# Kernel tuning notes

Measured on AMD Instinct MI355X. Metric: run time of the kernel, lower is better.

## Reference

```python
import jax, jax.numpy as jnp
import numpy as np

N = 20000      # total nodes
E = 320000     # edges (before self loops)
B = 8          # graphs in batch
F_IN = 100
HID = 256
HEADS = 4
DIMS = [(256, 256), (256, 128), (128, 64), (64, 32)]  # (in_dim, out_dim) per level
NEG_SLOPE = 0.2
LN_EPS = 1e-5


def _glorot(k, shape):
    fan = shape[0] + shape[-1]
    return jax.random.normal(k, shape, jnp.float32) * jnp.sqrt(2.0 / fan)


def setup_inputs() -> dict:
    key = jax.random.key(0)
    ks = jax.random.split(key, 32)
    inp = {}
    inp["x"] = jax.random.normal(ks[0], (N, F_IN), jnp.float32)
    inp["edge_index"] = jax.random.randint(ks[1], (2, E), 0, N)
    inp["batch"] = jnp.sort(jax.random.randint(ks[2], (N,), 0, B))
    inp["W_in"] = _glorot(ks[3], (F_IN, HID))
    inp["b_in"] = jnp.zeros((HID,), jnp.float32)
    i = 4
    for l, (di, do) in enumerate(DIMS):
        inp[f"W{l}"] = _glorot(ks[i], (di, HEADS * do)); i += 1
        inp[f"as{l}"] = _glorot(ks[i], (HEADS, do)); i += 1
        inp[f"ad{l}"] = _glorot(ks[i], (HEADS, do)); i += 1
        inp[f"b{l}"] = jnp.zeros((do,), jnp.float32)
        inp[f"g{l}"] = jnp.ones((do,), jnp.float32)
        inp[f"be{l}"] = jnp.zeros((do,), jnp.float32)
    inp["W_out"] = _glorot(ks[i], (DIMS[-1][1], 1))
    inp["b_out"] = jnp.zeros((1,), jnp.float32)
    return inp


def _gat(x, src, dst, W, a_s, a_d, b):
    # PyG GATConv, heads=HEADS, concat=False (head mean), bias after mean
    h = (x @ W).reshape(N, HEADS, -1)              # [N,H,C]
    al_s = (h * a_s).sum(-1)                        # [N,H]
    al_d = (h * a_d).sum(-1)                        # [N,H]
    e = jax.nn.leaky_relu(al_s[src] + al_d[dst], NEG_SLOPE)  # [Etot,H]
    m = jax.ops.segment_max(e, dst, num_segments=N)
    m = jnp.where(jnp.isfinite(m), m, 0.0)
    ex = jnp.exp(e - m[dst])
    den = jax.ops.segment_sum(ex, dst, num_segments=N)
    alpha = ex / (den[dst] + 1e-16)                 # segment softmax over incoming edges
    out = jax.ops.segment_sum(alpha[:, :, None] * h[src], dst, num_segments=N)
    return out.mean(axis=1) + b                     # [N,C]


def _ln(x, g, b):
    mu = x.mean(-1, keepdims=True)
    var = ((x - mu) ** 2).mean(-1, keepdims=True)
    return (x - mu) * jax.lax.rsqrt(var + LN_EPS) * g + b


def _forward(x, edge_index, batch, W_in, b_in, level_params, W_out, b_out):
    loop = jnp.arange(N)
    src = jnp.concatenate([edge_index[0], loop])    # add self loops (GATConv default)
    dst = jnp.concatenate([edge_index[1], loop])
    h = jax.nn.relu(x @ W_in + b_in)
    for (di, do), (W, a_s, a_d, b, g, be) in zip(DIMS, level_params):
        out = _gat(h, src, dst, W, a_s, a_d, b)
        out = jax.nn.relu(out)
        out = _ln(out, g, be)
        # dropout is identity in eval mode
        if di == do:
            out = out + h
        h = out
    cnt = jax.ops.segment_sum(jnp.ones((N,), h.dtype), batch, num_segments=B)
    pooled = jax.ops.segment_sum(h, batch, num_segments=B) / jnp.maximum(cnt, 1.0)[:, None]
    return (pooled @ W_out + b_out)[:, 0]           # [B]


def reference(x, edge_index, batch, W_in, b_in,
              W0, as0, ad0, b0, g0, be0,
              W1, as1, ad1, b1, g1, be1,
              W2, as2, ad2, b2, g2, be2,
              W3, as3, ad3, b3, g3, be3,
              W_out, b_out):
    level_params = [
        (W0, as0, ad0, b0, g0, be0),
        (W1, as1, ad1, b1, g1, be1),
        (W2, as2, ad2, b2, g2, be2),
        (W3, as3, ad3, b3, g3, be3),
    ]
    return _forward(x, edge_index, batch, W_in, b_in, level_params, W_out, b_out)
```

## Files before the change

### kernel.cpp

```cpp
#include <hip/hip_runtime.h>
#include <hip/hip_bf16.h>
#include <cstdint>

constexpr int NN   = 20000;
constexpr int NE   = 320000;
constexpr int ETOT = NE + NN;
constexpr int BG   = 8;
constexpr int FIN  = 100;
constexpr int HID  = 256;
constexpr int H    = 4;
constexpr float SLOPE  = 0.2f;
constexpr float LN_EPS = 1e-5f;

#define DEVFN __device__ __forceinline__

typedef __bf16 bf16x8 __attribute__((ext_vector_type(8)));
typedef float  f32x4  __attribute__((ext_vector_type(4)));
typedef float  f32x2  __attribute__((ext_vector_type(2)));

DEVFN float lrelu(float v) { return v > 0.f ? v : SLOPE * v; }
DEVFN ushort f2bf(float f) {
    unsigned u = __float_as_uint(f);
    return (ushort)((u + 0x7fffu + ((u >> 16) & 1u)) >> 16);
}
DEVFN float bf_lo(unsigned u) { return __uint_as_float(u << 16); }
DEVFN float bf_hi(unsigned u) { return __uint_as_float(u & 0xffff0000u); }
DEVFN float bf2f(unsigned u) { return __uint_as_float(u << 16); }

__global__ void zero_u32(uint32_t* __restrict__ p, int n) {
    int i = blockIdx.x * blockDim.x + threadIdx.x;
    if (i < n) p[i] = 0u;
}

__global__ void count_deg(const int* __restrict__ ei, int* __restrict__ deg) {
    int k = blockIdx.x * blockDim.x + threadIdx.x;
    if (k >= ETOT) return;
    int d = (k < NE) ? ei[NE + k] : (k - NE);
    atomicAdd(&deg[d], 1);
}

__global__ void scan_kernel(const int* __restrict__ deg, int* __restrict__ rowptr) {
    __shared__ int buf[1024];
    int carry = 0;
    for (int base = 0; base < NN; base += 1024) {
        int i = base + threadIdx.x;
        int v = (i < NN) ? deg[i] : 0;
        buf[threadIdx.x] = v;
        __syncthreads();
        for (int off = 1; off < 1024; off <<= 1) {
            int t = (threadIdx.x >= off) ? buf[threadIdx.x - off] : 0;
            __syncthreads();
            buf[threadIdx.x] += t;
            __syncthreads();
        }
        int incl = buf[threadIdx.x];
        if (i < NN) rowptr[i] = carry + incl - v;
        int total = buf[1023];
        __syncthreads();
        carry += total;
    }
    if (threadIdx.x == 0) rowptr[NN] = carry;
}

__global__ void scatter_edges(const int* __restrict__ ei, const int* __restrict__ rowptr,
                              int* __restrict__ fill, int* __restrict__ esrc) {
    int k = blockIdx.x * blockDim.x + threadIdx.x;
    if (k >= ETOT) return;
    int s, d;
    if (k < NE) { s = ei[k]; d = ei[NE + k]; }
    else        { s = k - NE; d = k - NE; }
    int pos = rowptr[d] + atomicAdd(&fill[d], 1);
    esrc[pos] = s;
}

template <int KS, int KP, int NC>
__global__ void convW(const float* __restrict__ W, ushort* __restrict__ Wt) {
    int id = blockIdx.x * blockDim.x + threadIdx.x;
    if (id >= NC * KP) return;
    int n = id / KP, k = id - n * KP;
    Wt[id] = (k < KS) ? f2bf(W[(size_t)k * NC + n]) : (ushort)0;
}

__global__ void convX(const float* __restrict__ x, ushort* __restrict__ xpad) {
    int id = blockIdx.x * blockDim.x + threadIdx.x;
    if (id >= NN * 128) return;
    int n = id >> 7, k = id & 127;
    xpad[id] = (k < FIN) ? f2bf(x[(size_t)n * FIN + k]) : (ushort)0;
}

template <int K, int NC, bool BR, bool AL>
__launch_bounds__(256)
__global__ void gemm_mfma(const ushort* __restrict__ A, const ushort* __restrict__ Wt,
                          const float* __restrict__ bias, void* __restrict__ Cout,
                          const float* __restrict__ a_s, const float* __restrict__ a_d,
                          float* __restrict__ al_s, float* __restrict__ al_d, int M) {
    constexpr int LDK = K + 8;
    constexpr int DO_AL = NC / H;
    __shared__ ushort As[64 * LDK];
    __shared__ ushort Bs[64 * LDK];
    const int row0 = blockIdx.x * 64;
    const int col0 = blockIdx.y * 64;
    const int tid = threadIdx.x;
    constexpr int CH = K / 8;
    for (int c = tid; c < 64 * CH; c += 256) {
        int r = c / CH, cc = c - r * CH;
        int gr = row0 + r;
        uint4 v = make_uint4(0u, 0u, 0u, 0u);
        if (gr < M) v = *(const uint4*)(A + (size_t)gr * K + cc * 8);
        *(uint4*)(&As[r * LDK + cc * 8]) = v;
        uint4 w = *(const uint4*)(Wt + (size_t)(col0 + r) * K + cc * 8);
        *(uint4*)(&Bs[r * LDK + cc * 8]) = w;
    }
    __syncthreads();
    const int wave = tid >> 6;
    const int lane = tid & 63;
    const int m = lane & 15;
    const int q = lane >> 4;
    f32x4 acc0 = {0.f, 0.f, 0.f, 0.f}, acc1 = acc0, acc2 = acc0, acc3 = acc0;
    const ushort* ap  = &As[(wave * 16 + m) * LDK + q * 8];
    const ushort* bp0 = &Bs[(0 * 16 + m) * LDK + q * 8];
    const ushort* bp1 = &Bs[(1 * 16 + m) * LDK + q * 8];
    const ushort* bp2 = &Bs[(2 * 16 + m) * LDK + q * 8];
    const ushort* bp3 = &Bs[(3 * 16 + m) * LDK + q * 8];
#pragma unroll
    for (int kk = 0; kk < K / 32; kk++) {
        bf16x8 a = *(const bf16x8*)(ap + kk * 32);
        acc0 = __builtin_amdgcn_mfma_f32_16x16x32_bf16(a, *(const bf16x8*)(bp0 + kk * 32), acc0, 0, 0, 0);
        acc1 = __builtin_amdgcn_mfma_f32_16x16x32_bf16(a, *(const bf16x8*)(bp1 + kk * 32), acc1, 0, 0, 0);
        acc2 = __builtin_amdgcn_mfma_f32_16x16x32_bf16(a, *(const bf16x8*)(bp2 + kk * 32), acc2, 0, 0, 0);
        acc3 = __builtin_amdgcn_mfma_f32_16x16x32_bf16(a, *(const bf16x8*)(bp3 + kk * 32), acc3, 0, 0, 0);
    }
    const int grow0 = row0 + wave * 16 + q * 4;
    if (!AL) {
        ushort* Cb = (ushort*)Cout + (size_t)grow0 * NC + col0 + m;
        float b0 = 0, b1 = 0, b2 = 0, b3 = 0;
        if (BR) {
            b0 = bias[col0 + m];      b1 = bias[col0 + m + 16];
            b2 = bias[col0 + m + 32]; b3 = bias[col0 + m + 48];
        }
#pragma unroll
        for (int r = 0; r < 4; r++) {
            if (grow0 + r < M) {
                float v0 = acc0[r], v1 = acc1[r], v2 = acc2[r], v3 = acc3[r];
                if (BR) {
                    v0 = fmaxf(v0 + b0, 0.f); v1 = fmaxf(v1 + b1, 0.f);
                    v2 = fmaxf(v2 + b2, 0.f); v3 = fmaxf(v3 + b3, 0.f);
                }
                Cb[(size_t)r * NC + 0]  = f2bf(v0);
                Cb[(size_t)r * NC + 16] = f2bf(v1);
                Cb[(size_t)r * NC + 32] = f2bf(v2);
                Cb[(size_t)r * NC + 48] = f2bf(v3);
            }
        }
    } else {
        uchar* Cb = (uchar*)Cout + (size_t)grow0 * NC + col0 + m;
#pragma unroll
        for (int r = 0; r < 4; r++) {
            if (grow0 + r < M) {
                int pk01 = __builtin_amdgcn_cvt_pk_fp8_f32(acc0[r], acc1[r], 0, false);
                int pk23 = __builtin_amdgcn_cvt_pk_fp8_f32(acc2[r], acc3[r], 0, false);
                Cb[(size_t)r * NC + 0]  = (uchar)(pk01 & 0xff);
                Cb[(size_t)r * NC + 16] = (uchar)((pk01 >> 8) & 0xff);
                Cb[(size_t)r * NC + 32] = (uchar)(pk23 & 0xff);
                Cb[(size_t)r * NC + 48] = (uchar)((pk23 >> 8) & 0xff);
            }
        }
        float asv[4], adv[4];
#pragma unroll
        for (int t = 0; t < 4; t++) {
            int gc = col0 + m + 16 * t;
            asv[t] = a_s[gc];
            adv[t] = a_d[gc];
        }
        const int h_lo = col0 / DO_AL;
        const int h_hi = (col0 + 32) / DO_AL;
#pragma unroll
        for (int r = 0; r < 4; r++) {
            float ps0 = acc0[r] * asv[0] + acc1[r] * asv[1];
            float ps1 = acc2[r] * asv[2] + acc3[r] * asv[3];
            float pd0 = acc0[r] * adv[0] + acc1[r] * adv[1];
            float pd1 = acc2[r] * adv[2] + acc3[r] * adv[3];
#pragma unroll
            for (int off = 1; off < 16; off <<= 1) {
                ps0 += __shfl_xor(ps0, off);
                ps1 += __shfl_xor(ps1, off);
                pd0 += __shfl_xor(pd0, off);
                pd1 += __shfl_xor(pd1, off);
            }
            if (m == 0 && grow0 + r < M) {
                if (h_lo == h_hi) {
                    atomicAdd(&al_s[(grow0 + r) * H + h_lo], ps0 + ps1);
                    atomicAdd(&al_d[(grow0 + r) * H + h_lo], pd0 + pd1);
                } else {
                    atomicAdd(&al_s[(grow0 + r) * H + h_lo], ps0);
                    atomicAdd(&al_s[(grow0 + r) * H + h_hi], ps1);
                    atomicAdd(&al_d[(grow0 + r) * H + h_lo], pd0);
                    atomicAdd(&al_d[(grow0 + r) * H + h_hi], pd1);
                }
            }
        }
    }
}

__global__ void softmax_csr(const int* __restrict__ rowptr, const int* __restrict__ esrc,
                            const float* __restrict__ al_s, const float* __restrict__ al_d,
                            float4* __restrict__ alpha) {
    int wid = (blockIdx.x * blockDim.x + threadIdx.x) >> 6;
    int lane = threadIdx.x & 63;
    if (wid >= NN) return;
    int p0 = rowptr[wid], p1 = rowptr[wid + 1];
    float4 d4 = ((const float4*)al_d)[wid];
    float m0 = -1e30f, m1 = -1e30f, m2 = -1e30f, m3 = -1e30f;
    for (int p = p0 + lane; p < p1; p += 64) {
        int s = esrc[p];
        float4 s4 = ((const float4*)al_s)[s];
        m0 = fmaxf(m0, lrelu(s4.x + d4.x));
        m1 = fmaxf(m1, lrelu(s4.y + d4.y));
        m2 = fmaxf(m2, lrelu(s4.z + d4.z));
        m3 = fmaxf(m3, lrelu(s4.w + d4.w));
    }
#pragma unroll
    for (int off = 32; off > 0; off >>= 1) {
        m0 = fmaxf(m0, __shfl_xor(m0, off));
        m1 = fmaxf(m1, __shfl_xor(m1, off));
        m2 = fmaxf(m2, __shfl_xor(m2, off));
        m3 = fmaxf(m3, __shfl_xor(m3, off));
    }
    float s0 = 0.f, s1 = 0.f, s2 = 0.f, s3 = 0.f;
    for (int p = p0 + lane; p < p1; p += 64) {
        int s = esrc[p];
        float4 s4 = ((const float4*)al_s)[s];
        s0 += __expf(lrelu(s4.x + d4.x) - m0);
        s1 += __expf(lrelu(s4.y + d4.y) - m1);
        s2 += __expf(lrelu(s4.z + d4.z) - m2);
        s3 += __expf(lrelu(s4.w + d4.w) - m3);
    }
#pragma unroll
    for (int off = 32; off > 0; off >>= 1) {
        s0 += __shfl_xor(s0, off);
        s1 += __shfl_xor(s1, off);
        s2 += __shfl_xor(s2, off);
        s3 += __shfl_xor(s3, off);
    }
    float i0 = 1.f / (s0 + 1e-16f), i1 = 1.f / (s1 + 1e-16f);
    float i2 = 1.f / (s2 + 1e-16f), i3 = 1.f / (s3 + 1e-16f);
    for (int p = p0 + lane; p < p1; p += 64) {
        int s = esrc[p];
        float4 s4 = ((const float4*)al_s)[s];
        alpha[p] = make_float4(__expf(lrelu(s4.x + d4.x) - m0) * i0,
                               __expf(lrelu(s4.y + d4.y) - m1) * i1,
                               __expf(lrelu(s4.z + d4.z) - m2) * i2,
                               __expf(lrelu(s4.w + d4.w) - m3) * i3);
    }
}

template <int DO, bool RESID>
__launch_bounds__(256)
__global__ void aggregate(const uchar* __restrict__ hproj, const int* __restrict__ rowptr,
                          const int* __restrict__ esrc, const float4* __restrict__ alpha,
                          const float* __restrict__ bias, const float* __restrict__ gamma,
                          const float* __restrict__ beta, const ushort* __restrict__ hprev,
                          ushort* __restrict__ hout) {
    constexpr int HDO = H * DO;
    constexpr int SL  = HDO / 16;
    constexpr int EPI = 256 / SL;
    constexpr int DO2 = DO / 2;
    __shared__ float part[256 * 16];
    __shared__ float red[256];
    const int n = blockIdx.x;
    const int tid = threadIdx.x;
    const int e = tid / SL;
    const int s = tid - e * SL;
    const int head = (s * 16) / DO;
    const int p0 = rowptr[n], p1 = rowptr[n + 1];
    const uint4* hp4 = (const uint4*)hproj;

    float acc[16];
#pragma unroll
    for (int j = 0; j < 16; j++) acc[j] = 0.f;

    int p = p0 + e;
    if (p < p1) {
        int src = esrc[p];
        float4 al4 = alpha[p];
        while (true) {
            int pn = p + EPI;
            bool more = (pn < p1);
            int srcn = 0;
            float4 aln = make_float4(0.f, 0.f, 0.f, 0.f);
            if (more) { srcn = esrc[pn]; aln = alpha[pn]; }
            uint4 v = hp4[(size_t)src * SL + s];
            float a = (head == 0) ? al4.x : (head == 1) ? al4.y : (head == 2) ? al4.z : al4.w;
            f32x2 d;
            d = __builtin_amdgcn_cvt_pk_f32_fp8(v.x, false); acc[0]  += a * d[0]; acc[1]  += a * d[1];
            d = __builtin_amdgcn_cvt_pk_f32_fp8(v.x, true);  acc[2]  += a * d[0]; acc[3]  += a * d[1];
            d = __builtin_amdgcn_cvt_pk_f32_fp8(v.y, false); acc[4]  += a * d[0]; acc[5]  += a * d[1];
            d = __builtin_amdgcn_cvt_pk_f32_fp8(v.y, true);  acc[6]  += a * d[0]; acc[7]  += a * d[1];
            d = __builtin_amdgcn_cvt_pk_f32_fp8(v.z, false); acc[8]  += a * d[0]; acc[9]  += a * d[1];
            d = __builtin_amdgcn_cvt_pk_f32_fp8(v.z, true);  acc[10] += a * d[0]; acc[11] += a * d[1];
            d = __builtin_amdgcn_cvt_pk_f32_fp8(v.w, false); acc[12] += a * d[0]; acc[13] += a * d[1];
            d = __builtin_amdgcn_cvt_pk_f32_fp8(v.w, true);  acc[14] += a * d[0]; acc[15] += a * d[1];
            if (!more) break;
            p = pn; src = srcn; al4 = aln;
        }
    }
#pragma unroll
    for (int j = 0; j < 16; j++) part[tid * 16 + j] = acc[j];
    __syncthreads();
    for (int c = tid; c < HDO; c += 256) {
        float v = part[c];
#pragma unroll
        for (int ee = 1; ee < EPI; ee++) v += part[ee * HDO + c];
        part[c] = v;
    }
    __syncthreads();
    float v0 = 0.f, v1 = 0.f;
    if (tid < DO2) {
#pragma unroll
        for (int h = 0; h < H; h++) {
            v0 += part[h * DO + 2 * tid];
            v1 += part[h * DO + 2 * tid + 1];
        }
        v0 = fmaxf(0.25f * v0 + bias[2 * tid], 0.f);
        v1 = fmaxf(0.25f * v1 + bias[2 * tid + 1], 0.f);
    }
    red[tid] = (tid < DO2) ? (v0 + v1) : 0.f;
    __syncthreads();
    for (int off = 128; off > 0; off >>= 1) {
        if (tid < off) red[tid] += red[tid + off];
        __syncthreads();
    }
    float mu = red[0] / DO;
    __syncthreads();
    float d0 = v0 - mu, d1 = v1 - mu;
    red[tid] = (tid < DO2) ? (d0 * d0 + d1 * d1) : 0.f;
    __syncthreads();
    for (int off = 128; off > 0; off >>= 1) {
        if (tid < off) red[tid] += red[tid + off];
        __syncthreads();
    }
    float rstd = rsqrtf(red[0] / DO + LN_EPS);
    if (tid < DO2) {
        float o0 = d0 * rstd * gamma[2 * tid]     + beta[2 * tid];
        float o1 = d1 * rstd * gamma[2 * tid + 1] + beta[2 * tid + 1];
        if (RESID) {
            unsigned pv = ((const unsigned*)(hprev + (size_t)n * DO))[tid];
            o0 += bf_lo(pv);
            o1 += bf_hi(pv);
        }
        unsigned ob = (unsigned)f2bf(o0) | ((unsigned)f2bf(o1) << 16);
        ((unsigned*)(hout + (size_t)n * DO))[tid] = ob;
    }
}

__global__ void pool_accum2(const ushort* __restrict__ h, const int* __restrict__ batch,
                            float* __restrict__ pooled, float* __restrict__ cnt) {
    __shared__ float lp[BG * 32];
    __shared__ float lc[BG];
    for (int i = threadIdx.x; i < BG * 32; i += blockDim.x) lp[i] = 0.f;
    if (threadIdx.x < BG) lc[threadIdx.x] = 0.f;
    __syncthreads();
    int c = threadIdx.x & 31;
    int rb = threadIdx.x >> 5;
    for (int n = blockIdx.x * 8 + rb; n < NN; n += gridDim.x * 8) {
        int b = batch[n];
        atomicAdd(&lp[b * 32 + c], bf2f((unsigned)h[(size_t)n * 32 + c]));
        if (c == 0) atomicAdd(&lc[b], 1.f);
    }
    __syncthreads();
    for (int i = threadIdx.x; i < BG * 32; i += blockDim.x) atomicAdd(&pooled[i], lp[i]);
    if (threadIdx.x < BG) atomicAdd(&cnt[threadIdx.x], lc[threadIdx.x]);
}

__global__ void final_out(const float* __restrict__ pooled, const float* __restrict__ cnt,
                          const float* __restrict__ Wo, const float* __restrict__ bo,
                          float* __restrict__ out) {
    int b = threadIdx.x;
    if (b < BG) {
        float inv = 1.f / fmaxf(cnt[b], 1.f);
        float acc = 0.f;
        for (int c = 0; c < 32; c++) acc += pooled[b * 32 + c] * inv * Wo[c];
        out[b] = acc + bo[0];
    }
}

extern "C" void kernel_launch(void* const* d_in, const int* in_sizes, int n_in,
                              void* d_out, int out_size, void* d_ws, size_t ws_size,
                              hipStream_t stream) {
    const float* x     = (const float*)d_in[0];
    const int*   ei    = (const int*)d_in[1];
    const int*   batch = (const int*)d_in[2];
    const float* Wi    = (const float*)d_in[3];
    const float* bi    = (const float*)d_in[4];
    const float* Wl[4]  = {(const float*)d_in[5],  (const float*)d_in[11], (const float*)d_in[17], (const float*)d_in[23]};
    const float* Asl[4] = {(const float*)d_in[6],  (const float*)d_in[12], (const float*)d_in[18], (const float*)d_in[24]};
    const float* Adl[4] = {(const float*)d_in[7],  (const float*)d_in[13], (const float*)d_in[19], (const float*)d_in[25]};
    const float* Bl[4]  = {(const float*)d_in[8],  (const float*)d_in[14], (const float*)d_in[20], (const float*)d_in[26]};
    const float* Gl[4]  = {(const float*)d_in[9],  (const float*)d_in[15], (const float*)d_in[21], (const float*)d_in[27]};
    const float* Bel[4] = {(const float*)d_in[10], (const float*)d_in[16], (const float*)d_in[22], (const float*)d_in[28]};
    const float* Wo = (const float*)d_in[29];
    const float* bo = (const float*)d_in[30];

    char* p = (char*)d_ws;
    auto take = [&](size_t bytes) -> void* {
        void* r = (void*)p;
        p += (bytes + 255) & ~(size_t)255;
        return r;
    };
    ushort*   hAbf   = (ushort*)take((size_t)NN * HID * 2);
    ushort*   hBbf   = (ushort*)take((size_t)NN * HID * 2);
    uchar*    hproj  = (uchar*)take((size_t)NN * H * HID);
    ushort*   xpad   = (ushort*)take((size_t)NN * 128 * 2);
    float*    al_s   = (float*)take((size_t)NN * H * 4);
    float*    al_d   = (float*)take((size_t)NN * H * 4);
    float4*   alpha  = (float4*)take((size_t)ETOT * 16);
    int*      deg    = (int*)take((size_t)NN * 4);
    int*      fill   = (int*)take((size_t)NN * 4);
    int*      rowptr = (int*)take((size_t)(NN + 1) * 4);
    int*      esrc   = (int*)take((size_t)ETOT * 4);
    float*    pooled = (float*)take((size_t)BG * 32 * 4);
    float*    cnt    = (float*)take((size_t)BG * 4);
    ushort*   wti    = (ushort*)take((size_t)256 * 128 * 2);
    ushort*   wt0    = (ushort*)take((size_t)1024 * 256 * 2);
    ushort*   wt1    = (ushort*)take((size_t)512 * 256 * 2);
    ushort*   wt2    = (ushort*)take((size_t)256 * 128 * 2);
    ushort*   wt3    = (ushort*)take((size_t)128 * 64 * 2);
    (void)ws_size; (void)n_in; (void)in_sizes; (void)out_size;

    const int ZB = 256;
    const int egrid = (ETOT + ZB - 1) / ZB;
    const int mtiles = (NN + 63) / 64;
    const int algrid = (2 * NN * H + ZB - 1) / ZB;

    zero_u32<<<(NN + ZB - 1) / ZB, ZB, 0, stream>>>((uint32_t*)deg, NN);
    zero_u32<<<(NN + ZB - 1) / ZB, ZB, 0, stream>>>((uint32_t*)fill, NN);
    zero_u32<<<2, ZB, 0, stream>>>((uint32_t*)pooled, BG * 32 + BG);

    convW<FIN, 128, 256><<<(256 * 128 + 255) / 256, 256, 0, stream>>>(Wi, wti);
    convW<256, 256, 1024><<<(1024 * 256 + 255) / 256, 256, 0, stream>>>(Wl[0], wt0);
    convW<256, 256, 512><<<(512 * 256 + 255) / 256, 256, 0, stream>>>(Wl[1], wt1);
    convW<128, 128, 256><<<(256 * 128 + 255) / 256, 256, 0, stream>>>(Wl[2], wt2);
    convW<64, 64, 128><<<(128 * 64 + 255) / 256, 256, 0, stream>>>(Wl[3], wt3);
    convX<<<(NN * 128 + 255) / 256, 256, 0, stream>>>(x, xpad);

    count_deg<<<egrid, ZB, 0, stream>>>(ei, deg);
    scan_kernel<<<1, 1024, 0, stream>>>(deg, rowptr);
    scatter_edges<<<egrid, ZB, 0, stream>>>(ei, rowptr, fill, esrc);

    const int sgrid = (NN * 64 + 255) / 256;

    gemm_mfma<128, 256, true, false><<<dim3(mtiles, 4), 256, 0, stream>>>(
        xpad, wti, bi, hAbf, nullptr, nullptr, nullptr, nullptr, NN);

    zero_u32<<<algrid, ZB, 0, stream>>>((uint32_t*)al_s, 2 * NN * H);
    gemm_mfma<256, 1024, false, true><<<dim3(mtiles, 16), 256, 0, stream>>>(
        hAbf, wt0, nullptr, hproj, Asl[0], Adl[0], al_s, al_d, NN);
    softmax_csr<<<sgrid, 256, 0, stream>>>(rowptr, esrc, al_s, al_d, alpha);
    aggregate<256, true><<<NN, 256, 0, stream>>>(hproj, rowptr, esrc, alpha,
                                                 Bl[0], Gl[0], Bel[0], hAbf, hBbf);
    zero_u32<<<algrid, ZB, 0, stream>>>((uint32_t*)al_s, 2 * NN * H);
    gemm_mfma<256, 512, false, true><<<dim3(mtiles, 8), 256, 0, stream>>>(
        hBbf, wt1, nullptr, hproj, Asl[1], Adl[1], al_s, al_d, NN);
    softmax_csr<<<sgrid, 256, 0, stream>>>(rowptr, esrc, al_s, al_d, alpha);
    aggregate<128, false><<<NN, 256, 0, stream>>>(hproj, rowptr, esrc, alpha,
                                                  Bl[1], Gl[1], Bel[1], nullptr, hAbf);
    zero_u32<<<algrid, ZB, 0, stream>>>((uint32_t*)al_s, 2 * NN * H);
    gemm_mfma<128, 256, false, true><<<dim3(mtiles, 4), 256, 0, stream>>>(
        hAbf, wt2, nullptr, hproj, Asl[2], Adl[2], al_s, al_d, NN);
    softmax_csr<<<sgrid, 256, 0, stream>>>(rowptr, esrc, al_s, al_d, alpha);
    aggregate<64, false><<<NN, 256, 0, stream>>>(hproj, rowptr, esrc, alpha,
                                                 Bl[2], Gl[2], Bel[2], nullptr, hBbf);
    zero_u32<<<algrid, ZB, 0, stream>>>((uint32_t*)al_s, 2 * NN * H);
    gemm_mfma<64, 128, false, true><<<dim3(mtiles, 2), 256, 0, stream>>>(
        hBbf, wt3, nullptr, hproj, Asl[3], Adl[3], al_s, al_d, NN);
    softmax_csr<<<sgrid, 256, 0, stream>>>(rowptr, esrc, al_s, al_d, alpha);
    aggregate<32, false><<<NN, 256, 0, stream>>>(hproj, rowptr, esrc, alpha,
                                                 Bl[3], Gl[3], Bel[3], nullptr, hAbf);

    pool_accum2<<<80, 256, 0, stream>>>(hAbf, batch, pooled, cnt);
    final_out<<<1, 64, 0, stream>>>(pooled, cnt, Wo, bo, (float*)d_out);
}
```

Measured before the change: 634.2 us.

## Fuse segment softmax into aggregation and batch setup conversions and zeroing

The separate softmax_csr kernel is removed. Each aggregate block now computes the per-head max over incoming edges, stages exponentials and source ids in shared memory chunks, accumulates unnormalized weighted features, and divides by the summed denominators at the end. This drops the alpha buffer's write and read and removes one launch per layer. Weight and input conversions are merged into a single conv_all kernel, and all zeroing (including per-layer al_s/al_d buffers) becomes one up-front launch. The cost is extra syncthreads and a max pass inside every aggregate block, and the partial-sum layout is changed to a padded transposed form.

```diff
diff --git a/kernel.cpp b/kernel.cpp
--- a/kernel.cpp
+++ b/kernel.cpp
@@ -73,19 +73,41 @@
     esrc[pos] = s;
 }
 
-template <int KS, int KP, int NC>
-__global__ void convW(const float* __restrict__ W, ushort* __restrict__ Wt) {
+constexpr int CXN  = NN * 128;
+constexpr int CWI  = 256 * 128;
+constexpr int CW0  = 1024 * 256;
+constexpr int CW1  = 512 * 256;
+constexpr int CW2  = 256 * 128;
+constexpr int CW3  = 128 * 64;
+constexpr int CTOT = CXN + CWI + CW0 + CW1 + CW2 + CW3;
+
+__global__ void conv_all(const float* __restrict__ x, const float* __restrict__ Wi,
+                         const float* __restrict__ W0, const float* __restrict__ W1,
+                         const float* __restrict__ W2, const float* __restrict__ W3,
+                         ushort* __restrict__ xpad, ushort* __restrict__ wti,
+                         ushort* __restrict__ wt0, ushort* __restrict__ wt1,
+                         ushort* __restrict__ wt2, ushort* __restrict__ wt3) {
     int id = blockIdx.x * blockDim.x + threadIdx.x;
-    if (id >= NC * KP) return;
-    int n = id / KP, k = id - n * KP;
-    Wt[id] = (k < KS) ? f2bf(W[(size_t)k * NC + n]) : (ushort)0;
-}
-
-__global__ void convX(const float* __restrict__ x, ushort* __restrict__ xpad) {
-    int id = blockIdx.x * blockDim.x + threadIdx.x;
-    if (id >= NN * 128) return;
-    int n = id >> 7, k = id & 127;
-    xpad[id] = (k < FIN) ? f2bf(x[(size_t)n * FIN + k]) : (ushort)0;
+    if (id < CXN) {
+        int n = id >> 7, k = id & 127;
+        xpad[id] = (k < FIN) ? f2bf(x[(size_t)n * FIN + k]) : (ushort)0;
+        return;
+    }
+    id -= CXN;
+    if (id < CWI) { int n = id / 128, k = id - n * 128;
+        wti[id] = (k < FIN) ? f2bf(Wi[(size_t)k * 256 + n]) : (ushort)0; return; }
+    id -= CWI;
+    if (id < CW0) { int n = id / 256, k = id - n * 256;
+        wt0[id] = f2bf(W0[(size_t)k * 1024 + n]); return; }
+    id -= CW0;
+    if (id < CW1) { int n = id / 256, k = id - n * 256;
+        wt1[id] = f2bf(W1[(size_t)k * 512 + n]); return; }
+    id -= CW1;
+    if (id < CW2) { int n = id / 128, k = id - n * 128;
+        wt2[id] = f2bf(W2[(size_t)k * 256 + n]); return; }
+    id -= CW2;
+    if (id < CW3) { int n = id / 64, k = id - n * 64;
+        wt3[id] = f2bf(W3[(size_t)k * 128 + n]); return; }
 }
 
 template <int K, int NC, bool BR, bool AL>
@@ -202,62 +224,11 @@
     }
 }
 
-__global__ void softmax_csr(const int* __restrict__ rowptr, const int* __restrict__ esrc,
-                            const float* __restrict__ al_s, const float* __restrict__ al_d,
-                            float4* __restrict__ alpha) {
-    int wid = (blockIdx.x * blockDim.x + threadIdx.x) >> 6;
-    int lane = threadIdx.x & 63;
-    if (wid >= NN) return;
-    int p0 = rowptr[wid], p1 = rowptr[wid + 1];
-    float4 d4 = ((const float4*)al_d)[wid];
-    float m0 = -1e30f, m1 = -1e30f, m2 = -1e30f, m3 = -1e30f;
-    for (int p = p0 + lane; p < p1; p += 64) {
-        int s = esrc[p];
-        float4 s4 = ((const float4*)al_s)[s];
-        m0 = fmaxf(m0, lrelu(s4.x + d4.x));
-        m1 = fmaxf(m1, lrelu(s4.y + d4.y));
-        m2 = fmaxf(m2, lrelu(s4.z + d4.z));
-        m3 = fmaxf(m3, lrelu(s4.w + d4.w));
-    }
-#pragma unroll
-    for (int off = 32; off > 0; off >>= 1) {
-        m0 = fmaxf(m0, __shfl_xor(m0, off));
-        m1 = fmaxf(m1, __shfl_xor(m1, off));
-        m2 = fmaxf(m2, __shfl_xor(m2, off));
-        m3 = fmaxf(m3, __shfl_xor(m3, off));
-    }
-    float s0 = 0.f, s1 = 0.f, s2 = 0.f, s3 = 0.f;
-    for (int p = p0 + lane; p < p1; p += 64) {
-        int s = esrc[p];
-        float4 s4 = ((const float4*)al_s)[s];
-        s0 += __expf(lrelu(s4.x + d4.x) - m0);
-        s1 += __expf(lrelu(s4.y + d4.y) - m1);
-        s2 += __expf(lrelu(s4.z + d4.z) - m2);
-        s3 += __expf(lrelu(s4.w + d4.w) - m3);
-    }
-#pragma unroll
-    for (int off = 32; off > 0; off >>= 1) {
-        s0 += __shfl_xor(s0, off);
-        s1 += __shfl_xor(s1, off);
-        s2 += __shfl_xor(s2, off);
-        s3 += __shfl_xor(s3, off);
-    }
-    float i0 = 1.f / (s0 + 1e-16f), i1 = 1.f / (s1 + 1e-16f);
-    float i2 = 1.f / (s2 + 1e-16f), i3 = 1.f / (s3 + 1e-16f);
-    for (int p = p0 + lane; p < p1; p += 64) {
-        int s = esrc[p];
-        float4 s4 = ((const float4*)al_s)[s];
-        alpha[p] = make_float4(__expf(lrelu(s4.x + d4.x) - m0) * i0,
-                               __expf(lrelu(s4.y + d4.y) - m1) * i1,
-                               __expf(lrelu(s4.z + d4.z) - m2) * i2,
-                               __expf(lrelu(s4.w + d4.w) - m3) * i3);
-    }
-}
-
 template <int DO, bool RESID>
 __launch_bounds__(256)
 __global__ void aggregate(const uchar* __restrict__ hproj, const int* __restrict__ rowptr,
-                          const int* __restrict__ esrc, const float4* __restrict__ alpha,
+                          const int* __restrict__ esrc,
+                          const float* __restrict__ al_s, const float* __restrict__ al_d,
                           const float* __restrict__ bias, const float* __restrict__ gamma,
                           const float* __restrict__ beta, const ushort* __restrict__ hprev,
                           ushort* __restrict__ hout) {
@@ -265,32 +236,76 @@
     constexpr int SL  = HDO / 16;
     constexpr int EPI = 256 / SL;
     constexpr int DO2 = DO / 2;
-    __shared__ float part[256 * 16];
-    __shared__ float red[256];
+    constexpr int CHK = 256;
+    __shared__ float4 exs[CHK];
+    __shared__ int    srcs[CHK];
+    __shared__ float  part[16 * 257];
+    __shared__ float  comb[HDO];
+    __shared__ float  red[256];
+    __shared__ float4 wred[4];
     const int n = blockIdx.x;
     const int tid = threadIdx.x;
-    const int e = tid / SL;
-    const int s = tid - e * SL;
-    const int head = (s * 16) / DO;
+    const int lane = tid & 63;
+    const int wave = tid >> 6;
     const int p0 = rowptr[n], p1 = rowptr[n + 1];
+    const float4 d4 = ((const float4*)al_d)[n];
+
+    float m0 = -1e30f, m1 = -1e30f, m2 = -1e30f, m3 = -1e30f;
+    for (int p = p0 + tid; p < p1; p += 256) {
+        int s = esrc[p];
+        float4 s4 = ((const float4*)al_s)[s];
+        m0 = fmaxf(m0, lrelu(s4.x + d4.x));
+        m1 = fmaxf(m1, lrelu(s4.y + d4.y));
+        m2 = fmaxf(m2, lrelu(s4.z + d4.z));
+        m3 = fmaxf(m3, lrelu(s4.w + d4.w));
+    }
+#pragma unroll
+    for (int off = 32; off > 0; off >>= 1) {
+        m0 = fmaxf(m0, __shfl_xor(m0, off));
+        m1 = fmaxf(m1, __shfl_xor(m1, off));
+        m2 = fmaxf(m2, __shfl_xor(m2, off));
+        m3 = fmaxf(m3, __shfl_xor(m3, off));
+    }
+    if (lane == 0) wred[wave] = make_float4(m0, m1, m2, m3);
+    __syncthreads();
+    {
+        float4 a = wred[0], b = wred[1], c = wred[2], d = wred[3];
+        m0 = fmaxf(fmaxf(a.x, b.x), fmaxf(c.x, d.x));
+        m1 = fmaxf(fmaxf(a.y, b.y), fmaxf(c.y, d.y));
+        m2 = fmaxf(fmaxf(a.z, b.z), fmaxf(c.z, d.z));
+        m3 = fmaxf(fmaxf(a.w, b.w), fmaxf(c.w, d.w));
+    }
+
+    const int e  = tid / SL;
+    const int sl = tid - e * SL;
+    const int head = (sl * 16) / DO;
     const uint4* hp4 = (const uint4*)hproj;
-
     float acc[16];
 #pragma unroll
     for (int j = 0; j < 16; j++) acc[j] = 0.f;
-
-    int p = p0 + e;
-    if (p < p1) {
-        int src = esrc[p];
-        float4 al4 = alpha[p];
-        while (true) {
-            int pn = p + EPI;
-            bool more = (pn < p1);
-            int srcn = 0;
-            float4 aln = make_float4(0.f, 0.f, 0.f, 0.f);
-            if (more) { srcn = esrc[pn]; aln = alpha[pn]; }
-            uint4 v = hp4[(size_t)src * SL + s];
-            float a = (head == 0) ? al4.x : (head == 1) ? al4.y : (head == 2) ? al4.z : al4.w;
+    float dn0 = 0.f, dn1 = 0.f, dn2 = 0.f, dn3 = 0.f;
+
+    for (int q = p0; q < p1; q += CHK) {
+        __syncthreads();
+        int idx = q + tid;
+        if (idx < p1) {
+            int sr = esrc[idx];
+            float4 s4 = ((const float4*)al_s)[sr];
+            float e0 = __expf(lrelu(s4.x + d4.x) - m0);
+            float e1 = __expf(lrelu(s4.y + d4.y) - m1);
+            float e2 = __expf(lrelu(s4.z + d4.z) - m2);
+            float e3 = __expf(lrelu(s4.w + d4.w) - m3);
+            exs[tid] = make_float4(e0, e1, e2, e3);
+            srcs[tid] = sr;
+            dn0 += e0; dn1 += e1; dn2 += e2; dn3 += e3;
+        }
+        __syncthreads();
+        int ne = min(CHK, p1 - q);
+        for (int t = e; t < ne; t += EPI) {
+            int src = srcs[t];
+            float4 ex4 = exs[t];
+            float a = (head == 0) ? ex4.x : (head == 1) ? ex4.y : (head == 2) ? ex4.z : ex4.w;
+            uint4 v = hp4[(size_t)src * SL + sl];
             f32x2 d;
             d = __builtin_amdgcn_cvt_pk_f32_fp8(v.x, false); acc[0]  += a * d[0]; acc[1]  += a * d[1];
             d = __builtin_amdgcn_cvt_pk_f32_fp8(v.x, true);  acc[2]  += a * d[0]; acc[3]  += a * d[1];
@@ -300,29 +315,47 @@
             d = __builtin_amdgcn_cvt_pk_f32_fp8(v.z, true);  acc[10] += a * d[0]; acc[11] += a * d[1];
             d = __builtin_amdgcn_cvt_pk_f32_fp8(v.w, false); acc[12] += a * d[0]; acc[13] += a * d[1];
             d = __builtin_amdgcn_cvt_pk_f32_fp8(v.w, true);  acc[14] += a * d[0]; acc[15] += a * d[1];
-            if (!more) break;
-            p = pn; src = srcn; al4 = aln;
-        }
-    }
-#pragma unroll
-    for (int j = 0; j < 16; j++) part[tid * 16 + j] = acc[j];
-    __syncthreads();
+        }
+    }
+
+#pragma unroll
+    for (int j = 0; j < 16; j++) part[j * 257 + tid] = acc[j];
+#pragma unroll
+    for (int off = 32; off > 0; off >>= 1) {
+        dn0 += __shfl_xor(dn0, off);
+        dn1 += __shfl_xor(dn1, off);
+        dn2 += __shfl_xor(dn2, off);
+        dn3 += __shfl_xor(dn3, off);
+    }
+    if (lane == 0) wred[wave] = make_float4(dn0, dn1, dn2, dn3);
+    __syncthreads();
+    float id0, id1, id2, id3;
+    {
+        float4 a = wred[0], b = wred[1], c = wred[2], d = wred[3];
+        id0 = 0.25f / (a.x + b.x + c.x + d.x + 1e-16f);
+        id1 = 0.25f / (a.y + b.y + c.y + d.y + 1e-16f);
+        id2 = 0.25f / (a.z + b.z + c.z + d.z + 1e-16f);
+        id3 = 0.25f / (a.w + b.w + c.w + d.w + 1e-16f);
+    }
     for (int c = tid; c < HDO; c += 256) {
-        float v = part[c];
-#pragma unroll
-        for (int ee = 1; ee < EPI; ee++) v += part[ee * HDO + c];
-        part[c] = v;
+        int s_ = c >> 4, j = c & 15;
+        float v = 0.f;
+#pragma unroll
+        for (int ee = 0; ee < EPI; ee++) v += part[j * 257 + ee * SL + s_];
+        int h = c / DO;
+        float invd = (h == 0) ? id0 : (h == 1) ? id1 : (h == 2) ? id2 : id3;
+        comb[c] = v * invd;
     }
     __syncthreads();
     float v0 = 0.f, v1 = 0.f;
     if (tid < DO2) {
 #pragma unroll
         for (int h = 0; h < H; h++) {
-            v0 += part[h * DO + 2 * tid];
-            v1 += part[h * DO + 2 * tid + 1];
-        }
-        v0 = fmaxf(0.25f * v0 + bias[2 * tid], 0.f);
-        v1 = fmaxf(0.25f * v1 + bias[2 * tid + 1], 0.f);
+            v0 += comb[h * DO + 2 * tid];
+            v1 += comb[h * DO + 2 * tid + 1];
+        }
+        v0 = fmaxf(v0 + bias[2 * tid], 0.f);
+        v1 = fmaxf(v1 + bias[2 * tid + 1], 0.f);
     }
     red[tid] = (tid < DO2) ? (v0 + v1) : 0.f;
     __syncthreads();
@@ -411,70 +444,55 @@
     ushort*   hBbf   = (ushort*)take((size_t)NN * HID * 2);
     uchar*    hproj  = (uchar*)take((size_t)NN * H * HID);
     ushort*   xpad   = (ushort*)take((size_t)NN * 128 * 2);
-    float*    al_s   = (float*)take((size_t)NN * H * 4);
-    float*    al_d   = (float*)take((size_t)NN * H * 4);
-    float4*   alpha  = (float4*)take((size_t)ETOT * 16);
+    int*      rowptr = (int*)take((size_t)(NN + 1) * 4);
+    int*      esrc   = (int*)take((size_t)ETOT * 4);
+    ushort*   wti    = (ushort*)take((size_t)CWI * 2);
+    ushort*   wt0    = (ushort*)take((size_t)CW0 * 2);
+    ushort*   wt1    = (ushort*)take((size_t)CW1 * 2);
+    ushort*   wt2    = (ushort*)take((size_t)CW2 * 2);
+    ushort*   wt3    = (ushort*)take((size_t)CW3 * 2);
+    char*     zbase  = p;
     int*      deg    = (int*)take((size_t)NN * 4);
     int*      fill   = (int*)take((size_t)NN * 4);
-    int*      rowptr = (int*)take((size_t)(NN + 1) * 4);
-    int*      esrc   = (int*)take((size_t)ETOT * 4);
     float*    pooled = (float*)take((size_t)BG * 32 * 4);
     float*    cnt    = (float*)take((size_t)BG * 4);
-    ushort*   wti    = (ushort*)take((size_t)256 * 128 * 2);
-    ushort*   wt0    = (ushort*)take((size_t)1024 * 256 * 2);
-    ushort*   wt1    = (ushort*)take((size_t)512 * 256 * 2);
-    ushort*   wt2    = (ushort*)take((size_t)256 * 128 * 2);
-    ushort*   wt3    = (ushort*)take((size_t)128 * 64 * 2);
+    float*    als[4], *ald[4];
+    for (int l = 0; l < 4; l++) {
+        als[l] = (float*)take((size_t)NN * H * 4);
+        ald[l] = (float*)take((size_t)NN * H * 4);
+    }
+    const int zcount = (int)((p - zbase) / 4);
     (void)ws_size; (void)n_in; (void)in_sizes; (void)out_size;
 
     const int ZB = 256;
     const int egrid = (ETOT + ZB - 1) / ZB;
     const int mtiles = (NN + 63) / 64;
-    const int algrid = (2 * NN * H + ZB - 1) / ZB;
-
-    zero_u32<<<(NN + ZB - 1) / ZB, ZB, 0, stream>>>((uint32_t*)deg, NN);
-    zero_u32<<<(NN + ZB - 1) / ZB, ZB, 0, stream>>>((uint32_t*)fill, NN);
-    zero_u32<<<2, ZB, 0, stream>>>((uint32_t*)pooled, BG * 32 + BG);
-
-    convW<FIN, 128, 256><<<(256 * 128 + 255) / 256, 256, 0, stream>>>(Wi, wti);
-    convW<256, 256, 1024><<<(1024 * 256 + 255) / 256, 256, 0, stream>>>(Wl[0], wt0);
-    convW<256, 256, 512><<<(512 * 256 + 255) / 256, 256, 0, stream>>>(Wl[1], wt1);
-    convW<128, 128, 256><<<(256 * 128 + 255) / 256, 256, 0, stream>>>(Wl[2], wt2);
-    convW<64, 64, 128><<<(128 * 64 + 255) / 256, 256, 0, stream>>>(Wl[3], wt3);
-    convX<<<(NN * 128 + 255) / 256, 256, 0, stream>>>(x, xpad);
-
+
+    zero_u32<<<(zcount + ZB - 1) / ZB, ZB, 0, stream>>>((uint32_t*)zbase, zcount);
+    conv_all<<<(CTOT + ZB - 1) / ZB, ZB, 0, stream>>>(x, Wi, Wl[0], Wl[1], Wl[2], Wl[3],
+                                                      xpad, wti, wt0, wt1, wt2, wt3);
     count_deg<<<egrid, ZB, 0, stream>>>(ei, deg);
     scan_kernel<<<1, 1024, 0, stream>>>(deg, rowptr);
     scatter_edges<<<egrid, ZB, 0, stream>>>(ei, rowptr, fill, esrc);
 
-    const int sgrid = (NN * 64 + 255) / 256;
-
     gemm_mfma<128, 256, true, false><<<dim3(mtiles, 4), 256, 0, stream>>>(
         xpad, wti, bi, hAbf, nullptr, nullptr, nullptr, nullptr, NN);
 
-    zero_u32<<<algrid, ZB, 0, stream>>>((uint32_t*)al_s, 2 * NN * H);
     gemm_mfma<256, 1024, false, true><<<dim3(mtiles, 16), 256, 0, stream>>>(
-        hAbf, wt0, nullptr, hproj, Asl[0], Adl[0], al_s, al_d, NN);
-    softmax_csr<<<sgrid, 256, 0, stream>>>(rowptr, esrc, al_s, al_d, alpha);
-    aggregate<256, true><<<NN, 256, 0, stream>>>(hproj, rowptr, esrc, alpha,
+        hAbf, wt0, nullptr, hproj, Asl[0], Adl[0], als[0], ald[0], NN);
+    aggregate<256, true><<<NN, 256, 0, stream>>>(hproj, rowptr, esrc, als[0], ald[0],
                                                  Bl[0], Gl[0], Bel[0], hAbf, hBbf);
-    zero_u32<<<algrid, ZB, 0, stream>>>((uint32_t*)al_s, 2 * NN * H);
     gemm_mfma<256, 512, false, true><<<dim3(mtiles, 8), 256, 0, stream>>>(
-        hBbf, wt1, nullptr, hproj, Asl[1], Adl[1], al_s, al_d, NN);
-    softmax_csr<<<sgrid, 256, 0, stream>>>(rowptr, esrc, al_s, al_d, alpha);
-    aggregate<128, false><<<NN, 256, 0, stream>>>(hproj, rowptr, esrc, alpha,
+        hBbf, wt1, nullptr, hproj, Asl[1], Adl[1], als[1], ald[1], NN);
+    aggregate<128, false><<<NN, 256, 0, stream>>>(hproj, rowptr, esrc, als[1], ald[1],
                                                   Bl[1], Gl[1], Bel[1], nullptr, hAbf);
-    zero_u32<<<algrid, ZB, 0, stream>>>((uint32_t*)al_s, 2 * NN * H);
     gemm_mfma<128, 256, false, true><<<dim3(mtiles, 4), 256, 0, stream>>>(
-        hAbf, wt2, nullptr, hproj, Asl[2], Adl[2], al_s, al_d, NN);
-    softmax_csr<<<sgrid, 256, 0, stream>>>(rowptr, esrc, al_s, al_d, alpha);
-    aggregate<64, false><<<NN, 256, 0, stream>>>(hproj, rowptr, esrc, alpha,
+        hAbf, wt2, nullptr, hproj, Asl[2], Adl[2], als[2], ald[2], NN);
+    aggregate<64, false><<<NN, 256, 0, stream>>>(hproj, rowptr, esrc, als[2], ald[2],
                                                  Bl[2], Gl[2], Bel[2], nullptr, hBbf);
-    zero_u32<<<algrid, ZB, 0, stream>>>((uint32_t*)al_s, 2 * NN * H);
     gemm_mfma<64, 128, false, true><<<dim3(mtiles, 2), 256, 0, stream>>>(
-        hBbf, wt3, nullptr, hproj, Asl[3], Adl[3], al_s, al_d, NN);
-    softmax_csr<<<sgrid, 256, 0, stream>>>(rowptr, esrc, al_s, al_d, alpha);
-    aggregate<32, false><<<NN, 256, 0, stream>>>(hproj, rowptr, esrc, alpha,
+        hBbf, wt3, nullptr, hproj, Asl[3], Adl[3], als[3], ald[3], NN);
+    aggregate<32, false><<<NN, 256, 0, stream>>>(hproj, rowptr, esrc, als[3], ald[3],
                                                  Bl[3], Gl[3], Bel[3], nullptr, hAbf);
 
     pool_accum2<<<80, 256, 0, stream>>>(hAbf, batch, pooled, cnt);
```

Result: slower. 723.4 us (+14.1%).
